# Performance work log

Hardware: AMD Instinct MI355X
Metric: run time of the kernel (lower is better)

## Reference

```python
import jax, jax.numpy as jnp
import numpy as np

D_MODEL = 1024
N_HEADS = 16
D_K = D_MODEL // N_HEADS
D_FF = 4096
B, S = 2, 2048
EPS = 1e-5


def setup_inputs() -> dict:
    key = jax.random.key(0)
    ks = jax.random.split(key, 16)
    sc = 0.02
    inp = {
        'x': jax.random.normal(ks[0], (B, S, D_MODEL), dtype=jnp.float32),
        'mask': jnp.ones((B, 1, 1, S), dtype=jnp.int32),
        'Wq': jax.random.normal(ks[1], (D_MODEL, D_MODEL), dtype=jnp.float32) * sc,
        'bq': jnp.zeros((D_MODEL,), dtype=jnp.float32),
        'Wk': jax.random.normal(ks[2], (D_MODEL, D_MODEL), dtype=jnp.float32) * sc,
        'bk': jnp.zeros((D_MODEL,), dtype=jnp.float32),
        'Wv': jax.random.normal(ks[3], (D_MODEL, D_MODEL), dtype=jnp.float32) * sc,
        'bv': jnp.zeros((D_MODEL,), dtype=jnp.float32),
        'Wo': jax.random.normal(ks[4], (D_MODEL, D_MODEL), dtype=jnp.float32) * sc,
        'bo': jnp.zeros((D_MODEL,), dtype=jnp.float32),
        'W1': jax.random.normal(ks[5], (D_MODEL, D_FF), dtype=jnp.float32) * sc,
        'b1': jnp.zeros((D_FF,), dtype=jnp.float32),
        'W2': jax.random.normal(ks[6], (D_FF, D_MODEL), dtype=jnp.float32) * sc,
        'b2': jnp.zeros((D_MODEL,), dtype=jnp.float32),
        'g1': jnp.ones((D_MODEL,), dtype=jnp.float32),
        'be1': jnp.zeros((D_MODEL,), dtype=jnp.float32),
        'g2': jnp.ones((D_MODEL,), dtype=jnp.float32),
        'be2': jnp.zeros((D_MODEL,), dtype=jnp.float32),
    }
    return inp


def _layernorm(x, g, b):
    mu = jnp.mean(x, axis=-1, keepdims=True)
    var = jnp.mean(jnp.square(x - mu), axis=-1, keepdims=True)
    return (x - mu) * jax.lax.rsqrt(var + EPS) * g + b


def _split_heads(x):
    b, s, _ = x.shape
    return x.reshape(b, s, N_HEADS, D_K).transpose(0, 2, 1, 3)  # [B,H,S,Dk]


def reference(x, mask, Wq, bq, Wk, bk, Wv, bv, Wo, bo, W1, b1, W2, b2, g1, be1, g2, be2):
    Q = _split_heads(x @ Wq + bq)
    K = _split_heads(x @ Wk + bk)
    V = _split_heads(x @ Wv + bv)
    scores = jnp.einsum('bhqd,bhkd->bhqk', Q, K) / jnp.sqrt(jnp.float32(D_K))
    scores = jnp.where(mask == 0, -jnp.inf, scores)
    attn = jax.nn.softmax(scores, axis=-1)
    ctx = jnp.einsum('bhqk,bhkd->bhqd', attn, V)
    ctx = ctx.transpose(0, 2, 1, 3).reshape(x.shape[0], x.shape[1], D_MODEL)
    attn_out = ctx @ Wo + bo
    h = _layernorm(x + attn_out, g1, be1)
    ff = jax.nn.relu(h @ W1 + b1) @ W2 + b2
    return _layernorm(h + ff, g2, be2)
```

## Files before the change

kernel.cpp:

```cpp
#include <hip/hip_runtime.h>
#include <hip/hip_bf16.h>

#define D_MODELC 1024
#define D_FFC    4096
#define N_HEADSC 16
#define BATCHC   2
#define SEQC     2048
#define M_TOK    (BATCHC*SEQC)

typedef __attribute__((ext_vector_type(4)))  float f32x4;
typedef __attribute__((ext_vector_type(16))) float f32x16;
typedef __attribute__((ext_vector_type(8)))  short s16x8;
using bf16_t = __hip_bfloat16;

static __device__ __forceinline__ unsigned short f2bf_u16(float f) {
  bf16_t h = __float2bfloat16(f);
  return __builtin_bit_cast(unsigned short, h);
}

static __device__ __forceinline__ unsigned int cvt_pk_bf16(float lo, float hi2) {
  unsigned int r;
  asm("v_cvt_pk_bf16_f32 %0, %1, %2" : "=v"(r) : "v"(lo), "v"(hi2));
  return r;
}

#define PSWAP(a, b) asm volatile("v_permlane32_swap_b32 %0, %1" : "+v"(a), "+v"(b))

#define ASYNC_COPY16(dst_lds, src_g) \
  __builtin_amdgcn_global_load_lds((const __attribute__((address_space(1))) void*)(src_g), \
                                   (__attribute__((address_space(3))) void*)(dst_lds), 16, 0, 0)

__global__ __launch_bounds__(256) void k_prep(
    const float* __restrict__ x,
    const float* __restrict__ Wq, const float* __restrict__ Wk,
    const float* __restrict__ Wv, const float* __restrict__ Wo,
    const float* __restrict__ W1, const float* __restrict__ W2,
    const float* __restrict__ bq, const float* __restrict__ bk,
    const float* __restrict__ bv,
    bf16_t* __restrict__ x16, bf16_t* __restrict__ wqkvT, bf16_t* __restrict__ woT,
    bf16_t* __restrict__ w1T, bf16_t* __restrict__ w2T, float* __restrict__ bqkv) {
  __shared__ float tile[32][33];
  const int bidx = blockIdx.x;
  const int tid = threadIdx.x;

  if (bidx < 12288) {
    const float* in;
    bf16_t* out;
    int R, C, bx, by;
    if (bidx < 4096) {
      const int z = bidx >> 10, t = bidx & 1023;
      in = (z == 0) ? Wq : (z == 1) ? Wk : (z == 2) ? Wv : Wo;
      out = (z == 0) ? wqkvT : (z == 1) ? wqkvT + 1024 * 1024
           : (z == 2) ? wqkvT + 2 * 1024 * 1024 : woT;
      R = 1024; C = 1024; bx = t & 31; by = t >> 5;
    } else if (bidx < 8192) {
      const int t = bidx - 4096;
      in = W1; out = w1T; R = 1024; C = 4096; bx = t & 127; by = t >> 7;
    } else {
      const int t = bidx - 8192;
      in = W2; out = w2T; R = 4096; C = 1024; bx = t & 31; by = t >> 5;
    }
    const int tx = tid & 31, ty = tid >> 5;
    const int c0 = bx * 32, r0 = by * 32;
#pragma unroll
    for (int i = 0; i < 4; ++i)
      tile[ty + i * 8][tx] = in[(size_t)(r0 + ty + i * 8) * C + c0 + tx];
    __syncthreads();
#pragma unroll
    for (int i = 0; i < 4; ++i)
      out[(size_t)(c0 + ty + i * 8) * R + r0 + tx] = __float2bfloat16(tile[tx][ty + i * 8]);
  } else if (bidx < 16384) {
    const int i = (bidx - 12288) * 256 + tid;
    float4 v = ((const float4*)x)[i];
    short4 o;
    o.x = (short)f2bf_u16(v.x);
    o.y = (short)f2bf_u16(v.y);
    o.z = (short)f2bf_u16(v.z);
    o.w = (short)f2bf_u16(v.w);
    ((short4*)x16)[i] = o;
  } else {
    const int i = (bidx - 16384) * 256 + tid;
    float v = (i < 1024) ? bq[i] : (i < 2048) ? bk[i - 1024] : bv[i - 2048];
    bqkv[i] = v;
  }
}

__global__ __launch_bounds__(512, 2) void k_gemm256(
    const bf16_t* __restrict__ A, const bf16_t* __restrict__ BT,
    const float* __restrict__ bias, bf16_t* __restrict__ Cout,
    int N, int K, int lda, int ldb, int ldc, int mode) {
  __shared__ __align__(16) bf16_t Ab[2][256][64];
  __shared__ __align__(16) bf16_t Bb[2][256][64];

  const int nbn = N / 256;
  const int nwg = gridDim.x;
  const int cpx = nwg >> 3;
  const int wg = (blockIdx.x & 7) * cpx + (blockIdx.x >> 3);
  const int mb = wg / nbn, nb = wg % nbn;
  const int row0 = mb * 256, col0 = nb * 256;

  const int tid = threadIdx.x;
  const int w = tid >> 6, lane = tid & 63;
  const int lr = lane & 15, lg = lane >> 4;
  const int wr = w >> 2, wc = w & 3;
  const int s7 = lr & 7;

#define STAGE256(buf, kt_)                                                            \
  {                                                                                   \
    const int k0_ = (kt_) * 64;                                                       \
    _Pragma("unroll")                                                                 \
    for (int i_ = 0; i_ < 4; ++i_) {                                                  \
      int c_ = tid + i_ * 512;                                                        \
      int row_ = c_ >> 3, sg_ = (c_ & 7) ^ (row_ & 7);                                \
      ASYNC_COPY16(&Ab[buf][0][0] + (size_t)c_ * 8,                                   \
                   A + (size_t)(row0 + row_) * lda + k0_ + sg_ * 8);                  \
    }                                                                                 \
    _Pragma("unroll")                                                                 \
    for (int i_ = 0; i_ < 4; ++i_) {                                                  \
      int c_ = tid + i_ * 512;                                                        \
      int row_ = c_ >> 3, sg_ = (c_ & 7) ^ (row_ & 7);                                \
      ASYNC_COPY16(&Bb[buf][0][0] + (size_t)c_ * 8,                                   \
                   BT + (size_t)(col0 + row_) * ldb + k0_ + sg_ * 8);                 \
    }                                                                                 \
  }

  f32x4 acc[8][4];
#pragma unroll
  for (int m = 0; m < 8; ++m)
#pragma unroll
    for (int n = 0; n < 4; ++n) acc[m][n] = (f32x4){0.f, 0.f, 0.f, 0.f};

  const int nt = K / 64;
  STAGE256(0, 0)
  STAGE256(1, 1)
  asm volatile("s_waitcnt vmcnt(8)" ::: "memory");
  __builtin_amdgcn_sched_barrier(0);
  __builtin_amdgcn_s_barrier();

  for (int t = 0; t < nt; ++t) {
    const int cur = t & 1;
    s16x8 a0[8], b0[4];
#pragma unroll
    for (int m = 0; m < 8; ++m)
      a0[m] = *(const s16x8*)(&Ab[cur][wr * 128 + m * 16 + lr][(lg ^ s7) * 8]);
#pragma unroll
    for (int n = 0; n < 4; ++n)
      b0[n] = *(const s16x8*)(&Bb[cur][wc * 64 + n * 16 + lr][(lg ^ s7) * 8]);
    __builtin_amdgcn_s_setprio(1);
#pragma unroll
    for (int m = 0; m < 8; ++m)
#pragma unroll
      for (int n = 0; n < 4; ++n)
        acc[m][n] = __builtin_amdgcn_mfma_f32_16x16x32_bf16(a0[m], b0[n], acc[m][n], 0, 0, 0);
    __builtin_amdgcn_s_setprio(0);
    s16x8 a1[8], b1[4];
#pragma unroll
    for (int m = 0; m < 8; ++m)
      a1[m] = *(const s16x8*)(&Ab[cur][wr * 128 + m * 16 + lr][((4 + lg) ^ s7) * 8]);
#pragma unroll
    for (int n = 0; n < 4; ++n)
      b1[n] = *(const s16x8*)(&Bb[cur][wc * 64 + n * 16 + lr][((4 + lg) ^ s7) * 8]);
    asm volatile("s_waitcnt lgkmcnt(0)" ::: "memory");
    __builtin_amdgcn_sched_barrier(0);
    __builtin_amdgcn_s_barrier();
    if (t + 2 < nt) STAGE256(cur, t + 2)
    __builtin_amdgcn_s_setprio(1);
#pragma unroll
    for (int m = 0; m < 8; ++m)
#pragma unroll
      for (int n = 0; n < 4; ++n)
        acc[m][n] = __builtin_amdgcn_mfma_f32_16x16x32_bf16(a1[m], b1[n], acc[m][n], 0, 0, 0);
    __builtin_amdgcn_s_setprio(0);
    if (t + 2 < nt) {
      asm volatile("s_waitcnt vmcnt(8)" ::: "memory");
    } else {
      asm volatile("s_waitcnt vmcnt(0)" ::: "memory");
    }
    __builtin_amdgcn_sched_barrier(0);
    __builtin_amdgcn_s_barrier();
  }

#pragma unroll
  for (int m = 0; m < 8; ++m) {
    int grow = row0 + wr * 128 + m * 16 + lg * 4;
#pragma unroll
    for (int n = 0; n < 4; ++n) {
      int gcol = col0 + wc * 64 + n * 16 + lr;
      float bv = bias[gcol];
      float cs = (mode == 3 && gcol < 1024) ? 0.18033688f : 1.f;
#pragma unroll
      for (int r = 0; r < 4; ++r) {
        float v = (acc[m][n][r] + bv) * cs;
        if (mode == 1) v = fmaxf(v, 0.f);
        Cout[(size_t)(grow + r) * ldc + gcol] = __float2bfloat16(v);
      }
    }
  }
#undef STAGE256
}

#define GBK 64

__global__ __launch_bounds__(256, 2) void k_gemm(
    const bf16_t* __restrict__ A, const bf16_t* __restrict__ BT,
    const float* __restrict__ bias,
    float* __restrict__ p0, float* __restrict__ p1,
    void* __restrict__ Cout, int M, int N, int K,
    int lda, int ldb, int ldc, int mode, int nsplit) {
  __shared__ __align__(16) bf16_t Asm[128 * GBK];
  __shared__ __align__(16) bf16_t Bsm[128 * GBK];

  const int nbn = N / 128;
  const int nwg = gridDim.x;
  const int cpx = nwg >> 3;
  int wg = (blockIdx.x & 7) * cpx + (blockIdx.x >> 3);
  int kslice = 0;
  if (nsplit == 2) { kslice = wg & 1; wg >>= 1; }
  const int mb = wg / nbn, nb = wg % nbn;
  const int row0 = mb * 128, col0 = nb * 128;
  A  += (size_t)kslice * K;
  BT += (size_t)kslice * K;

  const int tid = threadIdx.x;
  const int w = tid >> 6, lane = tid & 63;
  const int lr = lane & 15, lg = lane >> 4;
  const int wr = w >> 1, wc = w & 1;
  const int wbase = tid & 192;

  f32x4 acc[4][4];
#pragma unroll
  for (int m = 0; m < 4; ++m)
#pragma unroll
    for (int n = 0; n < 4; ++n) acc[m][n] = (f32x4){0.f, 0.f, 0.f, 0.f};

  for (int k0 = 0; k0 < K; k0 += GBK) {
    __syncthreads();
#pragma unroll
    for (int i = 0; i < 4; ++i) {
      int c = i * 256 + tid;
      int row = c >> 3;
      int sg = (c & 7) ^ (row & 7);
      ASYNC_COPY16(Asm + (size_t)(i * 256 + wbase) * 8,
                   A + (size_t)(row0 + row) * lda + k0 + sg * 8);
    }
#pragma unroll
    for (int i = 0; i < 4; ++i) {
      int c = i * 256 + tid;
      int row = c >> 3;
      int sg = (c & 7) ^ (row & 7);
      ASYNC_COPY16(Bsm + (size_t)(i * 256 + wbase) * 8,
                   BT + (size_t)(col0 + row) * ldb + k0 + sg * 8);
    }
    __syncthreads();
#pragma unroll
    for (int kst = 0; kst < 2; ++kst) {
      const int sl = ((kst * 4 + lg) ^ (lr & 7)) * 8;
      s16x8 af[4], bfr[4];
#pragma unroll
      for (int m = 0; m < 4; ++m)
        af[m] = *(const s16x8*)(Asm + (size_t)(wr * 64 + m * 16 + lr) * GBK + sl);
#pragma unroll
      for (int n = 0; n < 4; ++n)
        bfr[n] = *(const s16x8*)(Bsm + (size_t)(wc * 64 + n * 16 + lr) * GBK + sl);
#pragma unroll
      for (int m = 0; m < 4; ++m)
#pragma unroll
        for (int n = 0; n < 4; ++n)
          acc[m][n] = __builtin_amdgcn_mfma_f32_16x16x32_bf16(af[m], bfr[n], acc[m][n], 0, 0, 0);
    }
  }

  float* outf = (kslice == 0) ? p0 : p1;
  bf16_t* outh = (bf16_t*)Cout;
#pragma unroll
  for (int m = 0; m < 4; ++m) {
    int grow = row0 + wr * 64 + m * 16 + lg * 4;
#pragma unroll
    for (int n = 0; n < 4; ++n) {
      int gcol = col0 + wc * 64 + n * 16 + lr;
      float bv = (mode == 4) ? 0.f : bias[gcol];
      float cs = 1.f;
#pragma unroll
      for (int r = 0; r < 4; ++r) {
        float v = (acc[m][n][r] + bv) * cs;
        size_t idx = (size_t)(grow + r) * ldc + gcol;
        if (mode == 4) {
          outf[idx] = v;
        } else {
          if (mode == 1) v = fmaxf(v, 0.f);
          outh[idx] = __float2bfloat16(v);
        }
      }
    }
  }
}

__global__ __launch_bounds__(256, 4) void k_attn(
    const bf16_t* __restrict__ qkv, const int* __restrict__ mask,
    float* __restrict__ pA, float* __restrict__ pB,
    float* __restrict__ psA, float* __restrict__ psB) {
  const int bid = blockIdx.x;
  const int half = bid >> 9;
  const int inner = bid & 511;
  const int qt = inner & 15;
  const int h  = (inner >> 4) & 15;
  const int b  = inner >> 8;
  const int tid = threadIdx.x;
  const int w = tid >> 6, lane = tid & 63;
  const int l31 = lane & 31, hi = lane >> 5;
  const int wbase = tid & 192;

  __shared__ __align__(16) bf16_t Kl[2][64][64];
  __shared__ __align__(16) bf16_t Vl[2][4096];
  __shared__ __align__(16) float  mskf[2][68];

  const int tokb = b * SEQC;
  const int q0 = qt * 128 + w * 32;
  const int kb0 = half * (SEQC / 2);

  s16x8 qfrag[4];
  {
    const bf16_t* qp = qkv + (size_t)(tokb + q0 + l31) * 3072 + h * 64 + hi * 8;
#pragma unroll
    for (int s = 0; s < 4; ++s) qfrag[s] = *(const s16x8*)(qp + s * 16);
  }

  char* klc = (char*)&Kl[0][0][0];
  bf16_t* Vl0 = &Vl[0][0];
  const unsigned vbase =
      (unsigned)(size_t)(__attribute__((address_space(3))) bf16_t*)Vl0 + lane * 8;

  int vkey0, vd0, vkey1, vd1;
  {
    int c = tid, L = c >> 3;
    int f_ = L >> 4, t_ = (L >> 3) & 1, db_ = (L >> 2) & 1, h_ = (L >> 1) & 1, dl_ = L & 1;
    vkey0 = 16 * f_ + 8 * h_ + 4 * t_ + ((c & 7) >> 1);
    vd0 = ((db_ * 2 + dl_) << 4) + (c & 1) * 8;
  }
  {
    int c = tid + 256, L = c >> 3;
    int f_ = L >> 4, t_ = (L >> 3) & 1, db_ = (L >> 2) & 1, h_ = (L >> 1) & 1, dl_ = L & 1;
    vkey1 = 16 * f_ + 8 * h_ + 4 * t_ + ((c & 7) >> 1);
    vd1 = ((db_ * 2 + dl_) << 4) + (c & 1) * 8;
  }
  const bf16_t* srcV0 = qkv + (size_t)(tokb + kb0 + vkey0) * 3072 + 2048 + (size_t)h * 64 + vd0;
  const bf16_t* srcV1 = qkv + (size_t)(tokb + kb0 + vkey1) * 3072 + 2048 + (size_t)h * 64 + vd1;
  const int krow0 = ((w * 2 + 0) * 8) + (lane >> 3);
  const int krow1 = ((w * 2 + 1) * 8) + (lane >> 3);
  const bf16_t* srcK0 = qkv + (size_t)(tokb + kb0 + krow0) * 3072 + 1024 + (size_t)h * 64
                        + (((lane & 7) ^ (krow0 & 7)) * 8);
  const bf16_t* srcK1 = qkv + (size_t)(tokb + kb0 + krow1) * 3072 + 1024 + (size_t)h * 64
                        + (((lane & 7) ^ (krow1 & 7)) * 8);
  const int* mptr = mask + tokb + kb0 + lane;

  float mreg = 1.f;

#define STAGE_K(buf)                                                                  \
  {                                                                                   \
    ASYNC_COPY16(&Kl[buf][(w * 2 + 0) * 8][0], srcK0);                                \
    ASYNC_COPY16(&Kl[buf][(w * 2 + 1) * 8][0], srcK1);                                \
    srcK0 += 64 * 3072;                                                               \
    srcK1 += 64 * 3072;                                                               \
  }

#define STAGE_V(buf)                                                                  \
  {                                                                                   \
    ASYNC_COPY16(Vl0 + (size_t)(buf) * 4096 + (size_t)wbase * 8, srcV0);              \
    ASYNC_COPY16(Vl0 + (size_t)(buf) * 4096 + (size_t)(256 + wbase) * 8, srcV1);      \
    srcV0 += 64 * 3072;                                                               \
    srcV1 += 64 * 3072;                                                               \
  }

#define STAGE_M(buf)                                                                  \
  {                                                                                   \
    if (w == 0) {                                                                     \
      mreg = *mptr ? 1.f : 0.f;                                                       \
      mskf[buf][lane] = mreg;                                                         \
      unsigned long long z = __ballot(mreg == 0.f);                                   \
      if (lane == 0) mskf[buf][64] = (z == 0ull) ? 1.f : 0.f;                         \
    }                                                                                 \
    mptr += 64;                                                                       \
  }

  STAGE_K(0)
  STAGE_V(0)
  STAGE_M(0)

  f32x16 o[2];
#pragma unroll
  for (int d = 0; d < 2; ++d)
#pragma unroll
    for (int i = 0; i < 16; ++i) o[d][i] = 0.f;
  float psum = 0.f;

  __syncthreads();

  for (int kt = 0; kt < SEQC / 128; ++kt) {
    const int cur = kt & 1, nxt = cur ^ 1;
    const bool more = (kt < SEQC / 128 - 1);

    if (more) {
      STAGE_K(nxt)
      STAGE_V(nxt)
      STAGE_M(nxt)
    }

    f32x16 st[2];
#pragma unroll
    for (int kk = 0; kk < 2; ++kk)
#pragma unroll
      for (int i = 0; i < 16; ++i) st[kk][i] = 0.f;
#pragma unroll
    for (int step = 0; step < 4; ++step) {
#pragma unroll
      for (int kb2 = 0; kb2 < 2; ++kb2) {
        int key = kb2 * 32 + l31;
        int seg = (2 * step + hi) ^ (lane & 7);
        s16x8 kf = *(const s16x8*)(klc + cur * 8192 + key * 128 + seg * 16);
        st[kb2] = __builtin_amdgcn_mfma_f32_32x32x16_bf16(kf, qfrag[step], st[kb2], 0, 0, 0);
      }
    }

    const bool allv = (mskf[cur][64] != 0.f);
    s16x8 pf[4];
#pragma unroll
    for (int kb2 = 0; kb2 < 2; ++kb2) {
      float pa[16];
      if (allv) {
#pragma unroll
        for (int i = 0; i < 16; ++i) {
          float e = __builtin_exp2f(st[kb2][i]);
          pa[i] = e;
          psum += e;
        }
      } else {
#pragma unroll
        for (int g = 0; g < 4; ++g) {
          f32x4 mm = *(const f32x4*)((char*)&mskf[cur][0] + (kb2 * 128 + g * 32 + hi * 16));
#pragma unroll
          for (int rr = 0; rr < 4; ++rr) {
            float e = __builtin_exp2f(st[kb2][g * 4 + rr]) * mm[rr];
            pa[g * 4 + rr] = e;
            psum += e;
          }
        }
      }
      unsigned int wv[8];
#pragma unroll
      for (int u = 0; u < 8; ++u) wv[u] = cvt_pk_bf16(pa[2 * u], pa[2 * u + 1]);
      unsigned int a0 = wv[0], b0 = wv[2]; PSWAP(a0, b0);
      unsigned int a1 = wv[1], b1 = wv[3]; PSWAP(a1, b1);
      unsigned int a2 = wv[4], b2 = wv[6]; PSWAP(a2, b2);
      unsigned int a3 = wv[5], b3 = wv[7]; PSWAP(a3, b3);
      uint4 u0 = {a0, a1, b0, b1};
      uint4 u1 = {a2, a3, b2, b3};
      pf[kb2 * 2 + 0] = __builtin_bit_cast(s16x8, u0);
      pf[kb2 * 2 + 1] = __builtin_bit_cast(s16x8, u1);
    }

    const unsigned va = vbase + cur * 8192;
#pragma unroll
    for (int db = 0; db < 2; ++db) {
      ulong tr[4][2];
#pragma unroll
      for (int f = 0; f < 4; ++f)
        asm volatile("ds_read_b64_tr_b16 %0, %2 offset:%c3\n\t"
                     "ds_read_b64_tr_b16 %1, %2 offset:%c4"
                     : "=v"(tr[f][0]), "=v"(tr[f][1])
                     : "v"(va), "i"((f * 16 + db * 4) * 128), "i"((f * 16 + 8 + db * 4) * 128));
      asm volatile("s_waitcnt lgkmcnt(0)" ::: "memory");
      __builtin_amdgcn_sched_barrier(0);
#pragma unroll
      for (int f = 0; f < 4; ++f) {
        ulong2 uv = {tr[f][0], tr[f][1]};
        s16x8 vfr = __builtin_bit_cast(s16x8, uv);
        o[db] = __builtin_amdgcn_mfma_f32_32x32x16_bf16(pf[f], vfr, o[db], 0, 0, 0);
      }
    }

    __syncthreads();
  }

  psum += __shfl_xor(psum, 32);
  float* po = half ? pB : pA;
  float* ps = half ? psB : psA;
#pragma unroll
  for (int dblk = 0; dblk < 2; ++dblk)
#pragma unroll
    for (int r = 0; r < 16; ++r) {
      int qq = (r & 3) + 8 * (r >> 2) + 4 * hi;
      int tok = tokb + q0 + qq;
      po[(size_t)tok * 1024 + h * 64 + dblk * 32 + l31] = o[dblk][r];
    }
  if (hi == 0)
    ps[(size_t)(tokb + q0 + l31) * 16 + h] = psum;
#undef STAGE_K
#undef STAGE_V
#undef STAGE_M
}

__global__ __launch_bounds__(256) void k_attn_merge(
    const float* __restrict__ pA, const float* __restrict__ pB,
    const float* __restrict__ psA, const float* __restrict__ psB,
    bf16_t* __restrict__ ctx) {
  const int row = blockIdx.x, tid = threadIdx.x;
  const size_t base = (size_t)row * 1024;
  const float4 a = ((const float4*)(pA + base))[tid];
  const float4 b = ((const float4*)(pB + base))[tid];
  const int hh = tid >> 4;
  const float rs = psA[row * 16 + hh] + psB[row * 16 + hh];
  const float inv = 1.f / rs;
  short4 ob;
  ob.x = (short)f2bf_u16((a.x + b.x) * inv);
  ob.y = (short)f2bf_u16((a.y + b.y) * inv);
  ob.z = (short)f2bf_u16((a.z + b.z) * inv);
  ob.w = (short)f2bf_u16((a.w + b.w) * inv);
  ((short4*)(ctx + base))[tid] = ob;
}

__global__ __launch_bounds__(256) void k_ln_res2(
    const float* __restrict__ p0, const float* __restrict__ p1,
    const float* __restrict__ res, const float* __restrict__ bias,
    const float* __restrict__ g, const float* __restrict__ be,
    float* __restrict__ outf, bf16_t* __restrict__ outh) {
  const int row = blockIdx.x, tid = threadIdx.x;
  const size_t base = (size_t)row * D_MODELC;
  const float4 a  = ((const float4*)(p0 + base))[tid];
  const float4 bq = ((const float4*)(p1 + base))[tid];
  const float4 c  = ((const float4*)(res + base))[tid];
  const float4 bi = ((const float4*)bias)[tid];
  float4 v;
  v.x = a.x + bq.x + c.x + bi.x;
  v.y = a.y + bq.y + c.y + bi.y;
  v.z = a.z + bq.z + c.z + bi.z;
  v.w = a.w + bq.w + c.w + bi.w;
  float s1 = v.x + v.y + v.z + v.w;
  float s2 = v.x * v.x + v.y * v.y + v.z * v.z + v.w * v.w;
#pragma unroll
  for (int mm = 1; mm < 64; mm <<= 1) {
    s1 += __shfl_xor(s1, mm);
    s2 += __shfl_xor(s2, mm);
  }
  __shared__ float sa[4], sb[4];
  const int wv = tid >> 6;
  if ((tid & 63) == 0) { sa[wv] = s1; sb[wv] = s2; }
  __syncthreads();
  s1 = sa[0] + sa[1] + sa[2] + sa[3];
  s2 = sb[0] + sb[1] + sb[2] + sb[3];
  const float mu = s1 * (1.f / D_MODELC);
  const float var = s2 * (1.f / D_MODELC) - mu * mu;
  const float rsq = rsqrtf(var + 1e-5f);
  const float4 gg = ((const float4*)g)[tid];
  const float4 bb = ((const float4*)be)[tid];
  float4 oo;
  oo.x = (v.x - mu) * rsq * gg.x + bb.x;
  oo.y = (v.y - mu) * rsq * gg.y + bb.y;
  oo.z = (v.z - mu) * rsq * gg.z + bb.z;
  oo.w = (v.w - mu) * rsq * gg.w + bb.w;
  ((float4*)(outf + base))[tid] = oo;
  if (outh) {
    short4 ob;
    ob.x = (short)f2bf_u16(oo.x);
    ob.y = (short)f2bf_u16(oo.y);
    ob.z = (short)f2bf_u16(oo.z);
    ob.w = (short)f2bf_u16(oo.w);
    ((short4*)(outh + base))[tid] = ob;
  }
}

extern "C" void kernel_launch(void* const* d_in, const int* in_sizes, int n_in,
                              void* d_out, int out_size, void* d_ws, size_t ws_size,
                              hipStream_t stream) {
  (void)in_sizes; (void)n_in; (void)out_size; (void)ws_size;
  const float* x   = (const float*)d_in[0];
  const int* mask  = (const int*)d_in[1];
  const float* Wq  = (const float*)d_in[2];
  const float* bq  = (const float*)d_in[3];
  const float* Wk  = (const float*)d_in[4];
  const float* bk  = (const float*)d_in[5];
  const float* Wv  = (const float*)d_in[6];
  const float* bv  = (const float*)d_in[7];
  const float* Wo  = (const float*)d_in[8];
  const float* bo  = (const float*)d_in[9];
  const float* W1  = (const float*)d_in[10];
  const float* b1  = (const float*)d_in[11];
  const float* W2  = (const float*)d_in[12];
  const float* b2  = (const float*)d_in[13];
  const float* g1  = (const float*)d_in[14];
  const float* be1 = (const float*)d_in[15];
  const float* g2  = (const float*)d_in[16];
  const float* be2 = (const float*)d_in[17];

  char* ws = (char*)d_ws;
  const size_t D = D_MODELC, F = D_FFC, M = M_TOK;
  const size_t SZ_X16  = M * D * 2;
  const size_t SZ_QKV  = M * 3 * D * 2;
  bf16_t* x16   = (bf16_t*)ws;
  bf16_t* ff1   = (bf16_t*)ws;
  bf16_t* qkvb  = (bf16_t*)(ws + SZ_X16);
  size_t off = SZ_X16 + SZ_QKV;
  bf16_t* ctx   = (bf16_t*)(ws + off); off += M * D * 2;
  bf16_t* wqkvT = (bf16_t*)(ws + off); off += 3 * D * D * 2;
  bf16_t* woT   = (bf16_t*)(ws + off); off += D * D * 2;
  bf16_t* w1T   = (bf16_t*)(ws + off); off += D * F * 2;
  bf16_t* w2T   = (bf16_t*)(ws + off); off += D * F * 2;
  float*  partA = (float*)(ws + off);  off += M * D * 4;
  float*  hbuf  = (float*)(ws + off);  off += M * D * 4;
  bf16_t* h16   = (bf16_t*)(ws + off); off += M * D * 2;
  float*  partB = (float*)(ws + off);  off += M * D * 4;
  float*  bqkv  = (float*)(ws + off);  off += 3 * D * 4;
  float*  psA   = (float*)(ws + off);  off += M * 16 * 4;
  float*  psB   = (float*)(ws + off);  off += M * 16 * 4;

  k_prep<<<16396, 256, 0, stream>>>(x, Wq, Wk, Wv, Wo, W1, W2, bq, bk, bv,
                                    x16, wqkvT, woT, w1T, w2T, bqkv);

  k_gemm256<<<192, 512, 0, stream>>>(x16, wqkvT, bqkv, qkvb,
                                     3072, 1024, 1024, 1024, 3072, 3);

  k_attn<<<1024, 256, 0, stream>>>(qkvb, mask, partA, partB, psA, psB);
  k_attn_merge<<<4096, 256, 0, stream>>>(partA, partB, psA, psB, ctx);

  k_gemm<<<512, 256, 0, stream>>>(ctx, woT, nullptr, partA, partB, nullptr,
                                  4096, 1024, 512, 1024, 1024, 1024, 4, 2);
  k_ln_res2<<<4096, 256, 0, stream>>>(partA, partB, x, bo, g1, be1, hbuf, h16);

  k_gemm256<<<256, 512, 0, stream>>>(h16, w1T, b1, ff1,
                                     4096, 1024, 1024, 1024, 4096, 1);
  k_gemm<<<512, 256, 0, stream>>>(ff1, w2T, nullptr, partA, partB, nullptr,
                                  4096, 1024, 2048, 4096, 4096, 1024, 4, 2);
  k_ln_res2<<<4096, 256, 0, stream>>>(partA, partB, hbuf, b2, g2, be2, (float*)d_out, nullptr);
}
```

Measured before the change: 234.1 us.

## Store attention partials in bf16, remap block order, add MFMA priority hints

The attention kernel now writes its unnormalized split-key partial outputs as bf16 instead of fp32, and the merge kernel reads bf16. This halves the traffic for the partial buffers. Block index decoding is remapped so that neighbouring blocks share query tiles across heads, batches and halves, which may change cache locality and scheduling. s_setprio is raised around the MFMA sections to favour matrix issue across waves. Rounding the partials to bf16 before the merge adds a small amount of precision loss.

```diff
diff --git a/kernel.cpp b/kernel.cpp
--- a/kernel.cpp
+++ b/kernel.cpp
@@ -279,10 +279,9 @@
     for (int n = 0; n < 4; ++n) {
       int gcol = col0 + wc * 64 + n * 16 + lr;
       float bv = (mode == 4) ? 0.f : bias[gcol];
-      float cs = 1.f;
 #pragma unroll
       for (int r = 0; r < 4; ++r) {
-        float v = (acc[m][n][r] + bv) * cs;
+        float v = acc[m][n][r] + bv;
         size_t idx = (size_t)(grow + r) * ldc + gcol;
         if (mode == 4) {
           outf[idx] = v;
@@ -297,14 +296,14 @@
 
 __global__ __launch_bounds__(256, 4) void k_attn(
     const bf16_t* __restrict__ qkv, const int* __restrict__ mask,
-    float* __restrict__ pA, float* __restrict__ pB,
+    bf16_t* __restrict__ pA, bf16_t* __restrict__ pB,
     float* __restrict__ psA, float* __restrict__ psB) {
   const int bid = blockIdx.x;
-  const int half = bid >> 9;
-  const int inner = bid & 511;
-  const int qt = inner & 15;
-  const int h  = (inner >> 4) & 15;
-  const int b  = inner >> 8;
+  const int j = (bid & 7) + ((bid >> 7) << 3);
+  const int qt = (bid >> 3) & 15;
+  const int h = j & 15;
+  const int b = (j >> 4) & 1;
+  const int half = j >> 5;
   const int tid = threadIdx.x;
   const int w = tid >> 6, lane = tid & 63;
   const int l31 = lane & 31, hi = lane >> 5;
@@ -410,6 +409,7 @@
     for (int kk = 0; kk < 2; ++kk)
 #pragma unroll
       for (int i = 0; i < 16; ++i) st[kk][i] = 0.f;
+    __builtin_amdgcn_s_setprio(1);
 #pragma unroll
     for (int step = 0; step < 4; ++step) {
 #pragma unroll
@@ -420,6 +420,7 @@
         st[kb2] = __builtin_amdgcn_mfma_f32_32x32x16_bf16(kf, qfrag[step], st[kb2], 0, 0, 0);
       }
     }
+    __builtin_amdgcn_s_setprio(0);
 
     const bool allv = (mskf[cur][64] != 0.f);
     s16x8 pf[4];
@@ -470,19 +471,21 @@
                      : "v"(va), "i"((f * 16 + db * 4) * 128), "i"((f * 16 + 8 + db * 4) * 128));
       asm volatile("s_waitcnt lgkmcnt(0)" ::: "memory");
       __builtin_amdgcn_sched_barrier(0);
+      __builtin_amdgcn_s_setprio(1);
 #pragma unroll
       for (int f = 0; f < 4; ++f) {
         ulong2 uv = {tr[f][0], tr[f][1]};
         s16x8 vfr = __builtin_bit_cast(s16x8, uv);
         o[db] = __builtin_amdgcn_mfma_f32_32x32x16_bf16(pf[f], vfr, o[db], 0, 0, 0);
       }
+      __builtin_amdgcn_s_setprio(0);
     }
 
     __syncthreads();
   }
 
   psum += __shfl_xor(psum, 32);
-  float* po = half ? pB : pA;
+  bf16_t* po = half ? pB : pA;
   float* ps = half ? psB : psA;
 #pragma unroll
   for (int dblk = 0; dblk < 2; ++dblk)
@@ -490,7 +493,7 @@
     for (int r = 0; r < 16; ++r) {
       int qq = (r & 3) + 8 * (r >> 2) + 4 * hi;
       int tok = tokb + q0 + qq;
-      po[(size_t)tok * 1024 + h * 64 + dblk * 32 + l31] = o[dblk][r];
+      po[(size_t)tok * 1024 + h * 64 + dblk * 32 + l31] = __float2bfloat16(o[dblk][r]);
     }
   if (hi == 0)
     ps[(size_t)(tokb + q0 + l31) * 16 + h] = psum;
@@ -500,21 +503,23 @@
 }
 
 __global__ __launch_bounds__(256) void k_attn_merge(
-    const float* __restrict__ pA, const float* __restrict__ pB,
+    const bf16_t* __restrict__ pA, const bf16_t* __restrict__ pB,
     const float* __restrict__ psA, const float* __restrict__ psB,
     bf16_t* __restrict__ ctx) {
   const int row = blockIdx.x, tid = threadIdx.x;
   const size_t base = (size_t)row * 1024;
-  const float4 a = ((const float4*)(pA + base))[tid];
-  const float4 b = ((const float4*)(pB + base))[tid];
+  const short4 a4 = ((const short4*)(pA + base))[tid];
+  const short4 b4 = ((const short4*)(pB + base))[tid];
   const int hh = tid >> 4;
   const float rs = psA[row * 16 + hh] + psB[row * 16 + hh];
   const float inv = 1.f / rs;
+  const bf16_t* ae = (const bf16_t*)&a4;
+  const bf16_t* be = (const bf16_t*)&b4;
   short4 ob;
-  ob.x = (short)f2bf_u16((a.x + b.x) * inv);
-  ob.y = (short)f2bf_u16((a.y + b.y) * inv);
-  ob.z = (short)f2bf_u16((a.z + b.z) * inv);
-  ob.w = (short)f2bf_u16((a.w + b.w) * inv);
+  short* oe = (short*)&ob;
+#pragma unroll
+  for (int i = 0; i < 4; ++i)
+    oe[i] = (short)f2bf_u16((__bfloat162float(ae[i]) + __bfloat162float(be[i])) * inv);
   ((short4*)(ctx + base))[tid] = ob;
 }
 
@@ -618,8 +623,8 @@
   k_gemm256<<<192, 512, 0, stream>>>(x16, wqkvT, bqkv, qkvb,
                                      3072, 1024, 1024, 1024, 3072, 3);
 
-  k_attn<<<1024, 256, 0, stream>>>(qkvb, mask, partA, partB, psA, psB);
-  k_attn_merge<<<4096, 256, 0, stream>>>(partA, partB, psA, psB, ctx);
+  k_attn<<<1024, 256, 0, stream>>>(qkvb, mask, (bf16_t*)partA, (bf16_t*)partB, psA, psB);
+  k_attn_merge<<<4096, 256, 0, stream>>>((bf16_t*)partA, (bf16_t*)partB, psA, psB, ctx);
 
   k_gemm<<<512, 256, 0, stream>>>(ctx, woT, nullptr, partA, partB, nullptr,
                                   4096, 1024, 512, 1024, 1024, 1024, 4, 2);
```

Result: no change. 230.2 us (-1.7%).
